# Kernel tuning notes

Hardware: AMD Instinct MI355X
Metric: run time of the kernel (lower is better)

Reference implementation:

```python
import jax, jax.numpy as jnp
import numpy as np

NUM_HEADS = 8


def setup_inputs() -> dict:
    key = jax.random.key(0)
    ks = jax.random.split(key, 6)
    B, S, H = 2, 4096, 512
    Q = jax.random.normal(ks[0], (B, S, H), dtype=jnp.float32)
    K = jax.random.normal(ks[1], (B, S, H), dtype=jnp.float32)
    V = jax.random.normal(ks[2], (B, S, H), dtype=jnp.float32)
    risk_sigma = jax.random.uniform(ks[3], (B, 1), dtype=jnp.float32) * 0.2
    risk_lambda = jnp.array([2.0], dtype=jnp.float32)
    W_out = jax.random.normal(ks[4], (H, H), dtype=jnp.float32) * (1.0 / np.sqrt(H))
    b_out = jnp.zeros((H,), dtype=jnp.float32)
    return {"Q": Q, "K": K, "V": V, "risk_sigma": risk_sigma,
            "risk_lambda": risk_lambda, "W_out": W_out, "b_out": b_out}


def reference(Q, K, V, risk_sigma, risk_lambda, W_out, b_out):
    B, S, H = Q.shape
    nh = NUM_HEADS
    hd = H // nh
    # split heads: [B, S, nh, hd]
    q = Q.reshape(B, S, nh, hd)
    k = K.reshape(B, S, nh, hd)
    v = V.reshape(B, S, nh, hd)
    scale = 1.0 / jnp.sqrt(jnp.asarray(hd, dtype=Q.dtype))
    # [B, nh, S, S]
    scores = jnp.einsum('bshd,bthd->bhst', q, k) * scale
    # distance-based risk penalty
    pos = jnp.arange(S, dtype=Q.dtype)
    norm_dist = jnp.abs(pos[None, :] - pos[:, None]) / S  # [S, S]
    dist_sq = norm_dist ** 2
    sigma_c = jnp.clip(risk_sigma, 0.001, 0.2)            # [B, 1]
    sigma_n = (sigma_c - 0.001) / (0.2 - 0.001)
    lam = (risk_lambda / 10.0).reshape(())                 # scalar
    risk_term = lam * sigma_n[:, :, None, None] * dist_sq[None, None]  # [B,1,S,S]
    attn = jax.nn.softmax(scores - risk_term, axis=-1)
    ctx = jnp.einsum('bhst,bthd->bshd', attn, v).reshape(B, S, H)
    return ctx @ W_out.T + b_out
```

## Files before the change

### kernel.cpp

```cpp
#include <hip/hip_runtime.h>
#include <hip/hip_bf16.h>


#define S_LEN 4096
#define NHEAD 8
#define HD 64
#define HTOT 512

typedef __attribute__((ext_vector_type(8))) short short8;
typedef __attribute__((ext_vector_type(4))) float floatx4;
typedef __attribute__((ext_vector_type(2))) _Float16 half2v;

#if __has_builtin(__builtin_amdgcn_exp2f)
#define EXP2F(x) __builtin_amdgcn_exp2f(x)
#else
#define EXP2F(x) exp2f(x)
#endif

__device__ __forceinline__ unsigned pack_bf16(float a, float b) {
    unsigned ua = __builtin_bit_cast(unsigned, a) + 0x8000u;
    unsigned ub = __builtin_bit_cast(unsigned, b) + 0x8000u;
    return __builtin_amdgcn_perm(ub, ua, 0x07060302u);
}

__device__ __forceinline__ unsigned short f2bf(float x) {
    unsigned u = __builtin_bit_cast(unsigned, x) + 0x8000u;
    return (unsigned short)(u >> 16);
}

__device__ __forceinline__ void async16(const unsigned short* g, unsigned short* l) {
    __builtin_amdgcn_global_load_lds(
        (const __attribute__((address_space(1))) unsigned int*)g,
        (__attribute__((address_space(3))) unsigned int*)l, 16, 0, 0);
}

__global__ __launch_bounds__(256) void prep_kernel(
    const float* __restrict__ K, unsigned short* __restrict__ K16,
    const float* __restrict__ V, unsigned short* __restrict__ Vt)
{
    const int tid = threadIdx.x;
    if (blockIdx.x < 2048) {
        size_t i = ((size_t)blockIdx.x * 256 + tid) * 8;
        float4 a = *(const float4*)(K + i);
        float4 b = *(const float4*)(K + i + 4);
        unsigned o[4] = {pack_bf16(a.x, a.y), pack_bf16(a.z, a.w),
                         pack_bf16(b.x, b.y), pack_bf16(b.z, b.w)};
        *(short8*)(K16 + i) = *(short8*)o;
    } else {
        __shared__ unsigned short T[64 * 66];
        const int blk = blockIdx.x - 2048;
        const int st = blk & 63;
        const int bh = blk >> 6;
        const int b = bh >> 3, h = bh & 7;
        const float* src = V + ((size_t)b * S_LEN + st * 64) * HTOT + h * HD;
        for (int i = 0; i < 4; i++) {
            int idx = tid + i * 256;
            int s = idx >> 4, c4 = idx & 15;
            float4 v = *(const float4*)(src + (size_t)s * HTOT + c4 * 4);
            T[(c4 * 4 + 0) * 66 + s] = f2bf(v.x);
            T[(c4 * 4 + 1) * 66 + s] = f2bf(v.y);
            T[(c4 * 4 + 2) * 66 + s] = f2bf(v.z);
            T[(c4 * 4 + 3) * 66 + s] = f2bf(v.w);
        }
        __syncthreads();
        unsigned short* dst = Vt + ((size_t)bh * 64) * S_LEN + st * 64;
        for (int i = 0; i < 2; i++) {
            int idx = tid + i * 256;
            int d = idx >> 3, c8 = idx & 7;
            uint2 lo = *(const uint2*)&T[d * 66 + c8 * 8];
            uint2 hi = *(const uint2*)&T[d * 66 + c8 * 8 + 4];
            unsigned o[4] = {lo.x, lo.y, hi.x, hi.y};
            *(short8*)(dst + (size_t)d * S_LEN + c8 * 8) = *(short8*)o;
        }
    }
}

__global__ __launch_bounds__(256) void attn_kernel(
    const float* __restrict__ Q, const unsigned short* __restrict__ K16,
    const unsigned short* __restrict__ Vt,
    const float* __restrict__ risk_sigma, const float* __restrict__ risk_lambda,
    _Float16* __restrict__ Cpart, float* __restrict__ Lpart)
{
    __shared__ unsigned short QPsh[128 * 72];
    __shared__ unsigned short Ksh[64 * 64];
    __shared__ unsigned short Vsh[64 * 64];

    const int tid  = threadIdx.x;
    const int wave = tid >> 6;
    const int lane = tid & 63;
    const int quad = lane >> 4;
    const int ln   = lane & 15;
    const int sw   = ln & 7;

    const int bid = blockIdx.x;
    const int ks  = bid & 1;
    const int qt  = (bid >> 1) & 31;
    const int h   = (bid >> 6) & 7;
    const int b   = bid >> 9;
    const int qbase = qt * 128;

    float sig = risk_sigma[b];
    sig = fminf(fmaxf(sig, 0.001f), 0.2f);
    const float sn   = (sig - 0.001f) * (1.0f / 0.199f);
    const float coef = risk_lambda[0] * 0.1f * sn;
    const float nc2 = -coef * (1.0f / 4096.0f) * (1.0f / 4096.0f) * 1.4426950408889634f;
    const float qscale = 0.125f * 1.4426950408889634f;

    const float* Qb = Q + (size_t)b * S_LEN * HTOT + (size_t)h * HD;
    const unsigned short* Kb = K16 + (size_t)b * S_LEN * HTOT + (size_t)h * HD;
    const unsigned short* Vb = Vt + ((size_t)(b * 8 + h) * 64) * S_LEN;

    for (int i = 0; i < 8; i++) {
        int idx = tid + i * 256;
        int r = idx >> 4, c4 = idx & 15;
        float4 v = *(const float4*)(Qb + (size_t)(qbase + r) * HTOT + c4 * 4);
        uint2 o;
        o.x = pack_bf16(v.x * qscale, v.y * qscale);
        o.y = pack_bf16(v.z * qscale, v.w * qscale);
        *(uint2*)&QPsh[r * 72 + c4 * 4] = o;
    }
    __syncthreads();

    short8 qf[2][2];
    for (int nt = 0; nt < 2; nt++) {
        qf[nt][0] = *(const short8*)&QPsh[(wave * 32 + nt * 16 + ln) * 72 + quad * 8];
        qf[nt][1] = *(const short8*)&QPsh[(wave * 32 + nt * 16 + ln) * 72 + 32 + quad * 8];
    }
    unsigned short* Pw = &QPsh[wave * 32 * 72];

    floatx4 Oacc[2][4];
    for (int nt = 0; nt < 2; nt++)
        for (int dt = 0; dt < 4; dt++) Oacc[nt][dt] = (floatx4){0.f, 0.f, 0.f, 0.f};
    float lp[2] = {0.f, 0.f};

    const int qa = qbase + wave * 32;

    const int rl  = lane >> 3;
    const int c8g = ((lane & 7) ^ rl) << 3;

    for (int kt = ks * 32; kt < ks * 32 + 32; ++kt) {
        const int kbase = kt * 64;
        __syncthreads();
        {
            const unsigned short* gk = Kb + (size_t)(kbase + wave * 8 + rl) * HTOT + c8g;
            const unsigned short* gv = Vb + (size_t)(wave * 8 + rl) * S_LEN + kbase + c8g;
            async16(gk,              &Ksh[wave * 512 + lane * 8]);
            async16(gk + 32 * HTOT,  &Ksh[(wave + 4) * 512 + lane * 8]);
            async16(gv,              &Vsh[wave * 512 + lane * 8]);
            async16(gv + 32 * S_LEN, &Vsh[(wave + 4) * 512 + lane * 8]);
        }
        __syncthreads();

        const float dq = (float)(qa + ln - kbase);
        for (int jt = 0; jt < 4; jt++) {
            const int krow = (jt * 16 + ln) * 64;
            short8 ak0 = *(const short8*)&Ksh[krow + ((quad ^ sw) << 3)];
            short8 ak1 = *(const short8*)&Ksh[krow + (((quad + 4) ^ sw) << 3)];
            #pragma unroll
            for (int nt = 0; nt < 2; nt++) {
                floatx4 s = (floatx4){0.f, 0.f, 0.f, 0.f};
                s = __builtin_amdgcn_mfma_f32_16x16x32_bf16(ak0, qf[nt][0], s, 0, 0, 0);
                s = __builtin_amdgcn_mfma_f32_16x16x32_bf16(ak1, qf[nt][1], s, 0, 0, 0);
                float d = dq + (float)(nt * 16 - jt * 16 - quad * 4);
                float p[4];
                #pragma unroll
                for (int r = 0; r < 4; r++) {
                    float arg = __builtin_fmaf(nc2, d * d, s[r]);
                    p[r] = EXP2F(arg);
                    lp[nt] += p[r];
                    d -= 1.0f;
                }
                uint2 o;
                o.x = pack_bf16(p[0], p[1]);
                o.y = pack_bf16(p[2], p[3]);
                *(uint2*)&Pw[(nt * 16 + ln) * 72 + jt * 16 + quad * 4] = o;
            }
        }
        asm volatile("s_waitcnt lgkmcnt(0)" ::: "memory");
        __builtin_amdgcn_wave_barrier();

        short8 pf[2][2];
        for (int nt = 0; nt < 2; nt++) {
            pf[nt][0] = *(const short8*)&Pw[(nt * 16 + ln) * 72 + quad * 8];
            pf[nt][1] = *(const short8*)&Pw[(nt * 16 + ln) * 72 + 32 + quad * 8];
        }
        for (int dt = 0; dt < 4; dt++) {
            const int vrow = (dt * 16 + ln) * 64;
            short8 bv0 = *(const short8*)&Vsh[vrow + ((quad ^ sw) << 3)];
            short8 bv1 = *(const short8*)&Vsh[vrow + (((quad + 4) ^ sw) << 3)];
            #pragma unroll
            for (int nt = 0; nt < 2; nt++) {
                Oacc[nt][dt] = __builtin_amdgcn_mfma_f32_16x16x32_bf16(pf[nt][0], bv0, Oacc[nt][dt], 0, 0, 0);
                Oacc[nt][dt] = __builtin_amdgcn_mfma_f32_16x16x32_bf16(pf[nt][1], bv1, Oacc[nt][dt], 0, 0, 0);
            }
        }
    }

    _Float16* Cw = Cpart + (size_t)bid * (128 * 64);
    for (int nt = 0; nt < 2; nt++) {
        float l = lp[nt];
        l += __shfl_xor(l, 16, 64);
        l += __shfl_xor(l, 32, 64);
        if (quad == 0)
            Lpart[bid * 128 + wave * 32 + nt * 16 + ln] = l;
        float rl4 = 1.0f / l;
        float rlr[4];
        #pragma unroll
        for (int r = 0; r < 4; r++) rlr[r] = __shfl(rl4, quad * 4 + r, 64);
        for (int dt = 0; dt < 4; dt++)
            for (int r = 0; r < 4; r++) {
                int q = wave * 32 + nt * 16 + quad * 4 + r;
                Cw[q * 64 + dt * 16 + ln] = (_Float16)(Oacc[nt][dt][r] * rlr[r]);
            }
    }
}

__global__ __launch_bounds__(256) void combine_kernel(
    const _Float16* __restrict__ Cpart, const float* __restrict__ Lpart,
    unsigned short* __restrict__ ctx)
{
    const int t = threadIdx.x;
    const int tile = blockIdx.x;
    const int qt = tile & 31, h = (tile >> 5) & 7, b = tile >> 8;
    __shared__ float w0s[128], w1s[128];
    if (t < 128) {
        float l0 = Lpart[(tile * 2 + 0) * 128 + t];
        float l1 = Lpart[(tile * 2 + 1) * 128 + t];
        float inv = 1.0f / (l0 + l1);
        w0s[t] = l0 * inv;
        w1s[t] = l1 * inv;
    }
    __syncthreads();
    const _Float16* C0 = Cpart + (size_t)(tile * 2) * (128 * 64);
    const _Float16* C1 = C0 + 128 * 64;
    for (int i = 0; i < 8; i++) {
        int e = (i * 256 + t) * 4;
        int q = e >> 6, d = e & 63;
        half2v a0 = *(const half2v*)(C0 + e);
        half2v a1 = *(const half2v*)(C0 + e + 2);
        half2v b0 = *(const half2v*)(C1 + e);
        half2v b1 = *(const half2v*)(C1 + e + 2);
        float w0 = w0s[q], w1 = w1s[q];
        float v0 = w0 * (float)a0[0] + w1 * (float)b0[0];
        float v1 = w0 * (float)a0[1] + w1 * (float)b0[1];
        float v2 = w0 * (float)a1[0] + w1 * (float)b1[0];
        float v3 = w0 * (float)a1[1] + w1 * (float)b1[1];
        uint2 o;
        o.x = pack_bf16(v0, v1);
        o.y = pack_bf16(v2, v3);
        *(uint2*)&ctx[((size_t)b * S_LEN + qt * 128 + q) * HTOT + h * HD + d] = o;
    }
}

__global__ __launch_bounds__(256) void proj_kernel(
    const unsigned short* __restrict__ A,
    const float* __restrict__ W,
    const float* __restrict__ bias,
    float* __restrict__ out)
{
    __shared__ unsigned short Ash[64 * 40];
    __shared__ unsigned short Bsh[128 * 40];
    const int tid = threadIdx.x;
    const int wave = tid >> 6, lane = tid & 63, quad = lane >> 4, ln = lane & 15;
    const int wr = wave >> 1, wc = wave & 1;
    const int m0 = blockIdx.y * 64;
    const int nblock = blockIdx.x * 128;

    floatx4 acc[2][4];
    for (int i = 0; i < 2; i++)
        for (int j = 0; j < 4; j++) acc[i][j] = (floatx4){0.f, 0.f, 0.f, 0.f};

    for (int kt = 0; kt < 512 / 32; ++kt) {
        const int k0 = kt * 32;
        __syncthreads();
        {
            int r = tid >> 2, c8 = tid & 3;
            short8 v = *(const short8*)&A[(size_t)(m0 + r) * 512 + k0 + c8 * 8];
            *(short8*)&Ash[r * 40 + c8 * 8] = v;
        }
        for (int i = 0; i < 4; i++) {
            int idx = tid + i * 256;
            int r = idx >> 3, c4 = idx & 7;
            float4 v = *(const float4*)&W[(size_t)(nblock + r) * 512 + k0 + c4 * 4];
            uint2 o;
            o.x = pack_bf16(v.x, v.y);
            o.y = pack_bf16(v.z, v.w);
            *(uint2*)&Bsh[r * 40 + c4 * 4] = o;
        }
        __syncthreads();
        short8 af[2], bf[4];
        for (int i = 0; i < 2; i++)
            af[i] = *(const short8*)&Ash[(wr * 32 + i * 16 + ln) * 40 + quad * 8];
        for (int j = 0; j < 4; j++)
            bf[j] = *(const short8*)&Bsh[(wc * 64 + j * 16 + ln) * 40 + quad * 8];
        for (int i = 0; i < 2; i++)
            for (int j = 0; j < 4; j++)
                acc[i][j] = __builtin_amdgcn_mfma_f32_16x16x32_bf16(af[i], bf[j], acc[i][j], 0, 0, 0);
    }

    for (int i = 0; i < 2; i++) {
        int row = m0 + wr * 32 + i * 16 + quad * 4;
        for (int j = 0; j < 4; j++) {
            int col = nblock + wc * 64 + j * 16 + ln;
            float bv = bias[col];
            for (int r = 0; r < 4; r++)
                out[(size_t)(row + r) * 512 + col] = acc[i][j][r] + bv;
        }
    }
}

extern "C" void kernel_launch(void* const* d_in, const int* in_sizes, int n_in,
                              void* d_out, int out_size, void* d_ws, size_t ws_size,
                              hipStream_t stream) {
    const float* Q    = (const float*)d_in[0];
    const float* K    = (const float*)d_in[1];
    const float* V    = (const float*)d_in[2];
    const float* sig  = (const float*)d_in[3];
    const float* lam  = (const float*)d_in[4];
    const float* W    = (const float*)d_in[5];
    const float* bias = (const float*)d_in[6];

    unsigned short* ctx = (unsigned short*)d_ws;
    unsigned short* K16 = (unsigned short*)((char*)d_ws + (8u << 20));
    unsigned short* Vt  = (unsigned short*)((char*)d_ws + (16u << 20));
    float* Lpart        = (float*)((char*)d_ws + (24u << 20));
    _Float16* Cpart     = (_Float16*)d_out;
    float* out = (float*)d_out;

    prep_kernel<<<dim3(3072), dim3(256), 0, stream>>>(K, K16, V, Vt);
    attn_kernel<<<dim3(1024), dim3(256), 0, stream>>>(Q, K16, Vt, sig, lam, Cpart, Lpart);
    combine_kernel<<<dim3(512), dim3(256), 0, stream>>>(Cpart, Lpart, ctx);
    proj_kernel<<<dim3(4, 128), dim3(256), 0, stream>>>(ctx, W, bias, out);
}
```

Before: 232.8 us.

## Double-buffer K/V tiles, compute row sums via MFMA, fuse combine into projection

The attention loop now double-buffers K/V in shared memory, issuing the async copy for the next tile before computing the current one, with a single barrier per iteration. The first tile's copy overlaps the Q load. Softmax row sums are accumulated with extra MFMAs against a ones vector instead of scalar adds and shuffles. The separate combine kernel is removed: the projection kernel merges the two split-K partials and their weights while loading its A tile, which drops one launch and the ctx round trip. Costs are double the K/V shared memory, which may lower occupancy, and redundant partial merging across the four column blocks of the projection.

```diff
diff --git a/kernel.cpp b/kernel.cpp
--- a/kernel.cpp
+++ b/kernel.cpp
@@ -9,7 +9,7 @@
 
 typedef __attribute__((ext_vector_type(8))) short short8;
 typedef __attribute__((ext_vector_type(4))) float floatx4;
-typedef __attribute__((ext_vector_type(2))) _Float16 half2v;
+typedef __attribute__((ext_vector_type(8))) _Float16 half8;
 
 #if __has_builtin(__builtin_amdgcn_exp2f)
 #define EXP2F(x) __builtin_amdgcn_exp2f(x)
@@ -82,8 +82,8 @@
     _Float16* __restrict__ Cpart, float* __restrict__ Lpart)
 {
     __shared__ unsigned short QPsh[128 * 72];
-    __shared__ unsigned short Ksh[64 * 64];
-    __shared__ unsigned short Vsh[64 * 64];
+    __shared__ unsigned short Ksh[2][64 * 64];
+    __shared__ unsigned short Vsh[2][64 * 64];
 
     const int tid  = threadIdx.x;
     const int wave = tid >> 6;
@@ -110,6 +110,18 @@
     const unsigned short* Kb = K16 + (size_t)b * S_LEN * HTOT + (size_t)h * HD;
     const unsigned short* Vb = Vt + ((size_t)(b * 8 + h) * 64) * S_LEN;
 
+    const int rl  = lane >> 3;
+    const int c8g = ((lane & 7) ^ rl) << 3;
+    auto dma = [&](int buf, int kbase) {
+        const unsigned short* gk = Kb + (size_t)(kbase + wave * 8 + rl) * HTOT + c8g;
+        const unsigned short* gv = Vb + (size_t)(wave * 8 + rl) * S_LEN + kbase + c8g;
+        async16(gk,              &Ksh[buf][wave * 512 + lane * 8]);
+        async16(gk + 32 * HTOT,  &Ksh[buf][(wave + 4) * 512 + lane * 8]);
+        async16(gv,              &Vsh[buf][wave * 512 + lane * 8]);
+        async16(gv + 32 * S_LEN, &Vsh[buf][(wave + 4) * 512 + lane * 8]);
+    };
+
+    dma(0, ks * 2048);
     for (int i = 0; i < 8; i++) {
         int idx = tid + i * 256;
         int r = idx >> 4, c4 = idx & 15;
@@ -128,34 +140,29 @@
     }
     unsigned short* Pw = &QPsh[wave * 32 * 72];
 
-    floatx4 Oacc[2][4];
-    for (int nt = 0; nt < 2; nt++)
+    const short sone = (short)0x3F80;
+    const short8 ones = {sone, sone, sone, sone, sone, sone, sone, sone};
+
+    floatx4 Oacc[2][4], Lacc[2];
+    for (int nt = 0; nt < 2; nt++) {
+        Lacc[nt] = (floatx4){0.f, 0.f, 0.f, 0.f};
         for (int dt = 0; dt < 4; dt++) Oacc[nt][dt] = (floatx4){0.f, 0.f, 0.f, 0.f};
-    float lp[2] = {0.f, 0.f};
+    }
 
     const int qa = qbase + wave * 32;
 
-    const int rl  = lane >> 3;
-    const int c8g = ((lane & 7) ^ rl) << 3;
-
-    for (int kt = ks * 32; kt < ks * 32 + 32; ++kt) {
-        const int kbase = kt * 64;
-        __syncthreads();
-        {
-            const unsigned short* gk = Kb + (size_t)(kbase + wave * 8 + rl) * HTOT + c8g;
-            const unsigned short* gv = Vb + (size_t)(wave * 8 + rl) * S_LEN + kbase + c8g;
-            async16(gk,              &Ksh[wave * 512 + lane * 8]);
-            async16(gk + 32 * HTOT,  &Ksh[(wave + 4) * 512 + lane * 8]);
-            async16(gv,              &Vsh[wave * 512 + lane * 8]);
-            async16(gv + 32 * S_LEN, &Vsh[(wave + 4) * 512 + lane * 8]);
-        }
-        __syncthreads();
+    for (int kt = 0; kt < 32; ++kt) {
+        const int kbase = ks * 2048 + kt * 64;
+        const int cur = kt & 1;
+        if (kt < 31) dma(1 - cur, kbase + 64);
+        const unsigned short* Kc = Ksh[cur];
+        const unsigned short* Vc = Vsh[cur];
 
         const float dq = (float)(qa + ln - kbase);
         for (int jt = 0; jt < 4; jt++) {
             const int krow = (jt * 16 + ln) * 64;
-            short8 ak0 = *(const short8*)&Ksh[krow + ((quad ^ sw) << 3)];
-            short8 ak1 = *(const short8*)&Ksh[krow + (((quad + 4) ^ sw) << 3)];
+            short8 ak0 = *(const short8*)&Kc[krow + ((quad ^ sw) << 3)];
+            short8 ak1 = *(const short8*)&Kc[krow + (((quad + 4) ^ sw) << 3)];
             #pragma unroll
             for (int nt = 0; nt < 2; nt++) {
                 floatx4 s = (floatx4){0.f, 0.f, 0.f, 0.f};
@@ -167,7 +174,6 @@
                 for (int r = 0; r < 4; r++) {
                     float arg = __builtin_fmaf(nc2, d * d, s[r]);
                     p[r] = EXP2F(arg);
-                    lp[nt] += p[r];
                     d -= 1.0f;
                 }
                 uint2 o;
@@ -186,102 +192,98 @@
         }
         for (int dt = 0; dt < 4; dt++) {
             const int vrow = (dt * 16 + ln) * 64;
-            short8 bv0 = *(const short8*)&Vsh[vrow + ((quad ^ sw) << 3)];
-            short8 bv1 = *(const short8*)&Vsh[vrow + (((quad + 4) ^ sw) << 3)];
+            short8 bv0 = *(const short8*)&Vc[vrow + ((quad ^ sw) << 3)];
+            short8 bv1 = *(const short8*)&Vc[vrow + (((quad + 4) ^ sw) << 3)];
             #pragma unroll
             for (int nt = 0; nt < 2; nt++) {
                 Oacc[nt][dt] = __builtin_amdgcn_mfma_f32_16x16x32_bf16(pf[nt][0], bv0, Oacc[nt][dt], 0, 0, 0);
                 Oacc[nt][dt] = __builtin_amdgcn_mfma_f32_16x16x32_bf16(pf[nt][1], bv1, Oacc[nt][dt], 0, 0, 0);
             }
         }
+        #pragma unroll
+        for (int nt = 0; nt < 2; nt++) {
+            Lacc[nt] = __builtin_amdgcn_mfma_f32_16x16x32_bf16(pf[nt][0], ones, Lacc[nt], 0, 0, 0);
+            Lacc[nt] = __builtin_amdgcn_mfma_f32_16x16x32_bf16(pf[nt][1], ones, Lacc[nt], 0, 0, 0);
+        }
+        __syncthreads();
     }
 
     _Float16* Cw = Cpart + (size_t)bid * (128 * 64);
     for (int nt = 0; nt < 2; nt++) {
-        float l = lp[nt];
-        l += __shfl_xor(l, 16, 64);
-        l += __shfl_xor(l, 32, 64);
-        if (quad == 0)
-            Lpart[bid * 128 + wave * 32 + nt * 16 + ln] = l;
-        float rl4 = 1.0f / l;
-        float rlr[4];
+        if (ln == 0) {
+            #pragma unroll
+            for (int r = 0; r < 4; r++)
+                Lpart[bid * 128 + wave * 32 + nt * 16 + quad * 4 + r] = Lacc[nt][r];
+        }
+        float rl4[4];
         #pragma unroll
-        for (int r = 0; r < 4; r++) rlr[r] = __shfl(rl4, quad * 4 + r, 64);
+        for (int r = 0; r < 4; r++) rl4[r] = 1.0f / Lacc[nt][r];
         for (int dt = 0; dt < 4; dt++)
+            #pragma unroll
             for (int r = 0; r < 4; r++) {
                 int q = wave * 32 + nt * 16 + quad * 4 + r;
-                Cw[q * 64 + dt * 16 + ln] = (_Float16)(Oacc[nt][dt][r] * rlr[r]);
+                Cw[q * 64 + dt * 16 + ln] = (_Float16)(Oacc[nt][dt][r] * rl4[r]);
             }
     }
 }
 
-__global__ __launch_bounds__(256) void combine_kernel(
+__global__ __launch_bounds__(256) void projc_kernel(
     const _Float16* __restrict__ Cpart, const float* __restrict__ Lpart,
-    unsigned short* __restrict__ ctx)
-{
-    const int t = threadIdx.x;
-    const int tile = blockIdx.x;
-    const int qt = tile & 31, h = (tile >> 5) & 7, b = tile >> 8;
-    __shared__ float w0s[128], w1s[128];
-    if (t < 128) {
-        float l0 = Lpart[(tile * 2 + 0) * 128 + t];
-        float l1 = Lpart[(tile * 2 + 1) * 128 + t];
-        float inv = 1.0f / (l0 + l1);
-        w0s[t] = l0 * inv;
-        w1s[t] = l1 * inv;
-    }
-    __syncthreads();
-    const _Float16* C0 = Cpart + (size_t)(tile * 2) * (128 * 64);
-    const _Float16* C1 = C0 + 128 * 64;
-    for (int i = 0; i < 8; i++) {
-        int e = (i * 256 + t) * 4;
-        int q = e >> 6, d = e & 63;
-        half2v a0 = *(const half2v*)(C0 + e);
-        half2v a1 = *(const half2v*)(C0 + e + 2);
-        half2v b0 = *(const half2v*)(C1 + e);
-        half2v b1 = *(const half2v*)(C1 + e + 2);
-        float w0 = w0s[q], w1 = w1s[q];
-        float v0 = w0 * (float)a0[0] + w1 * (float)b0[0];
-        float v1 = w0 * (float)a0[1] + w1 * (float)b0[1];
-        float v2 = w0 * (float)a1[0] + w1 * (float)b1[0];
-        float v3 = w0 * (float)a1[1] + w1 * (float)b1[1];
-        uint2 o;
-        o.x = pack_bf16(v0, v1);
-        o.y = pack_bf16(v2, v3);
-        *(uint2*)&ctx[((size_t)b * S_LEN + qt * 128 + q) * HTOT + h * HD + d] = o;
-    }
-}
-
-__global__ __launch_bounds__(256) void proj_kernel(
-    const unsigned short* __restrict__ A,
-    const float* __restrict__ W,
-    const float* __restrict__ bias,
+    const float* __restrict__ W, const float* __restrict__ bias,
     float* __restrict__ out)
 {
     __shared__ unsigned short Ash[64 * 40];
     __shared__ unsigned short Bsh[128 * 40];
+    __shared__ float2 Lw[8][64];
+
     const int tid = threadIdx.x;
     const int wave = tid >> 6, lane = tid & 63, quad = lane >> 4, ln = lane & 15;
     const int wr = wave >> 1, wc = wave & 1;
     const int m0 = blockIdx.y * 64;
-    const int nblock = blockIdx.x * 128;
+    const int nb = blockIdx.x * 128;
+    const int b = m0 >> 12, qt = (m0 >> 7) & 31, qoff = m0 & 127;
+
+    for (int i = 0; i < 2; i++) {
+        int e = tid + i * 256;
+        int hh = e >> 6, r = e & 63;
+        int tile = (b * 8 + hh) * 32 + qt;
+        float l0 = Lpart[(size_t)(tile * 2 + 0) * 128 + qoff + r];
+        float l1 = Lpart[(size_t)(tile * 2 + 1) * 128 + qoff + r];
+        float inv = 1.0f / (l0 + l1);
+        Lw[hh][r] = (float2){l0 * inv, l1 * inv};
+    }
 
     floatx4 acc[2][4];
     for (int i = 0; i < 2; i++)
         for (int j = 0; j < 4; j++) acc[i][j] = (floatx4){0.f, 0.f, 0.f, 0.f};
 
-    for (int kt = 0; kt < 512 / 32; ++kt) {
+    const int ar = tid >> 2, ac8 = tid & 3;
+
+    for (int kt = 0; kt < 16; ++kt) {
         const int k0 = kt * 32;
+        const int h = k0 >> 6, d0 = k0 & 63;
         __syncthreads();
         {
-            int r = tid >> 2, c8 = tid & 3;
-            short8 v = *(const short8*)&A[(size_t)(m0 + r) * 512 + k0 + c8 * 8];
-            *(short8*)&Ash[r * 40 + c8 * 8] = v;
+            int tile = (b * 8 + h) * 32 + qt;
+            const _Float16* C0 = Cpart + (size_t)(tile * 2) * (128 * 64)
+                                 + (size_t)(qoff + ar) * 64 + d0 + ac8 * 8;
+            const _Float16* C1 = C0 + 128 * 64;
+            half8 a0 = *(const half8*)C0;
+            half8 a1 = *(const half8*)C1;
+            float2 w = Lw[h][ar];
+            unsigned o[4];
+            #pragma unroll
+            for (int k = 0; k < 4; k++) {
+                float v0 = w.x * (float)a0[2 * k]     + w.y * (float)a1[2 * k];
+                float v1 = w.x * (float)a0[2 * k + 1] + w.y * (float)a1[2 * k + 1];
+                o[k] = pack_bf16(v0, v1);
+            }
+            *(short8*)&Ash[ar * 40 + ac8 * 8] = *(short8*)o;
         }
         for (int i = 0; i < 4; i++) {
             int idx = tid + i * 256;
             int r = idx >> 3, c4 = idx & 7;
-            float4 v = *(const float4*)&W[(size_t)(nblock + r) * 512 + k0 + c4 * 4];
+            float4 v = *(const float4*)&W[(size_t)(nb + r) * 512 + k0 + c4 * 4];
             uint2 o;
             o.x = pack_bf16(v.x, v.y);
             o.y = pack_bf16(v.z, v.w);
@@ -301,8 +303,9 @@
     for (int i = 0; i < 2; i++) {
         int row = m0 + wr * 32 + i * 16 + quad * 4;
         for (int j = 0; j < 4; j++) {
-            int col = nblock + wc * 64 + j * 16 + ln;
+            int col = nb + wc * 64 + j * 16 + ln;
             float bv = bias[col];
+            #pragma unroll
             for (int r = 0; r < 4; r++)
                 out[(size_t)(row + r) * 512 + col] = acc[i][j][r] + bv;
         }
@@ -320,15 +323,13 @@
     const float* W    = (const float*)d_in[5];
     const float* bias = (const float*)d_in[6];
 
-    unsigned short* ctx = (unsigned short*)d_ws;
-    unsigned short* K16 = (unsigned short*)((char*)d_ws + (8u << 20));
-    unsigned short* Vt  = (unsigned short*)((char*)d_ws + (16u << 20));
-    float* Lpart        = (float*)((char*)d_ws + (24u << 20));
-    _Float16* Cpart     = (_Float16*)d_out;
+    unsigned short* K16 = (unsigned short*)d_ws;
+    unsigned short* Vt  = (unsigned short*)((char*)d_ws + (8u << 20));
+    _Float16* Cpart     = (_Float16*)((char*)d_ws + (16u << 20));
+    float* Lpart        = (float*)((char*)d_ws + (32u << 20));
     float* out = (float*)d_out;
 
     prep_kernel<<<dim3(3072), dim3(256), 0, stream>>>(K, K16, V, Vt);
     attn_kernel<<<dim3(1024), dim3(256), 0, stream>>>(Q, K16, Vt, sig, lam, Cpart, Lpart);
-    combine_kernel<<<dim3(512), dim3(256), 0, stream>>>(Cpart, Lpart, ctx);
-    proj_kernel<<<dim3(4, 128), dim3(256), 0, stream>>>(ctx, W, bias, out);
-}
+    projc_kernel<<<dim3(4, 128), dim3(256), 0, stream>>>(Cpart, Lpart, W, bias, out);
+}
```

After: 233.8 us. No clear change (+0.4%).
